# Kernel optimization log

Measured on AMD Instinct MI355X. Metric: run time of the kernel, lower is better.

The kernel has to match this reference:

```python
import jax, jax.numpy as jnp
import numpy as np

V, D, H, L_GNN = 50000, 256, 256, 4
B, NODES_PER_G, L, OUT = 16, 4000, 512, 256
N = B * NODES_PER_G            # 64000 total nodes
E = N * 16                     # 1,024,000 edges (avg degree 16)


def setup_inputs() -> dict:
    key = jax.random.key(0)
    ks = jax.random.split(key, 14)
    s = 0.02  # param init scale
    # per-graph local indices, offset into the flat node array (mirrors the
    # indices[...] + sum(x_len[:i]) reconstruction in the torch code)
    local = jax.random.randint(ks[3], (B, L), 0, NODES_PER_G)
    offsets = (jnp.arange(B, dtype=jnp.int32) * NODES_PER_G)[:, None]
    return {
        "x": jax.random.randint(ks[0], (N,), 0, V, dtype=jnp.int32),
        "edge_index": jax.random.randint(ks[1], (2, E), 0, N, dtype=jnp.int32),
        "edge_weight": jax.random.uniform(ks[2], (E,), jnp.float32),
        "gather_idx": (local + offsets).astype(jnp.int32),
        "mask": jnp.ones((B, L), dtype=bool),
        "encoder_embed": jax.random.normal(ks[4], (B, L, H), jnp.float32),
        "emb": jax.random.normal(ks[5], (V, D), jnp.float32) * s,
        "ggc_w": jax.random.normal(ks[6], (L_GNN, H, H), jnp.float32) * s,
        "w_ih": jax.random.normal(ks[7], (3 * H, H), jnp.float32) * s,
        "w_hh": jax.random.normal(ks[8], (3 * H, H), jnp.float32) * s,
        "b_ih": jnp.zeros((3 * H,), jnp.float32),
        "b_hh": jnp.zeros((3 * H,), jnp.float32),
        "out_w": jax.random.normal(ks[9], (OUT, 2 * H), jnp.float32) * s,
        "out_b": jnp.zeros((OUT,), jnp.float32),
    }


def _gru_cell(m, h, w_ih, w_hh, b_ih, b_hh):
    # torch.nn.GRUCell, gate order (r, z, n)
    gi = m @ w_ih.T + b_ih          # [N, 3H]
    gh = h @ w_hh.T + b_hh
    i_r, i_z, i_n = jnp.split(gi, 3, axis=-1)
    h_r, h_z, h_n = jnp.split(gh, 3, axis=-1)
    r = jax.nn.sigmoid(i_r + h_r)
    z = jax.nn.sigmoid(i_z + h_z)
    n = jnp.tanh(i_n + r * h_n)
    return (1.0 - z) * n + z * h


def reference(x, edge_index, edge_weight, gather_idx, mask, encoder_embed,
              emb, ggc_w, w_ih, w_hh, b_ih, b_hh, out_w, out_b):
    src, dst = edge_index[0], edge_index[1]  # PyG: aggregate x_j at target i
    h = emb[x]                                # [N, H] (dropout=0 -> identity)
    for i in range(L_GNN):                    # GatedGraphConv
        m = h @ ggc_w[i]                      # [N, H]
        msg = m[src] * edge_weight[:, None]   # [E, H]
        agg = jax.ops.segment_sum(msg, dst, num_segments=N)
        h = _gru_cell(agg, h, w_ih, w_hh, b_ih, b_hh)
    # gather per-graph node outputs and zero-pad to max_node_len
    out = h[gather_idx] * mask[:, :, None].astype(h.dtype)  # [B, L, H]
    out = jnp.concatenate([out, encoder_embed], axis=-1)    # [B, L, 2H]
    return out @ out_w.T + out_b                            # [B, L, OUT]
```

## Files before the change

kernel.cpp:

```cpp
#include <hip/hip_runtime.h>
#include <hip/hip_bf16.h>

typedef __hip_bfloat16 bf16;
typedef unsigned short u16;
typedef __attribute__((ext_vector_type(8))) short s8v;
typedef __attribute__((ext_vector_type(4))) float f4v;

#define MFMA16(a, b, c) __builtin_amdgcn_mfma_f32_16x16x32_bf16((a), (b), (c), 0, 0, 0)

__device__ __forceinline__ float b2f(bf16 v) { return __bfloat162float(v); }
__device__ __forceinline__ float sigm(float x) { return 1.0f / (1.0f + __expf(-x)); }
__device__ __forceinline__ float u2f(u16 u) {
  union { float f; unsigned int i; } v; v.i = ((unsigned int)u) << 16; return v.f;
}
__device__ __forceinline__ u16 f2u(float f) {
  bf16 b = __float2bfloat16(f);
  union { bf16 b; u16 u; } v; v.b = b; return v.u;
}

__device__ __forceinline__ void gl16(void* lds, const void* g) {
  __builtin_amdgcn_global_load_lds(
      (const __attribute__((address_space(1))) unsigned int*)g,
      (__attribute__((address_space(3))) unsigned int*)lds, 16, 0, 0);
}

__global__ __launch_bounds__(256) void k_cast(const float* __restrict__ s,
                                              bf16* __restrict__ d, int n) {
  int i = blockIdx.x * 256 + threadIdx.x;
  if (i < n) d[i] = __float2bfloat16(s[i]);
}

__global__ __launch_bounds__(256) void k_embed(const int* __restrict__ x,
                                               const float* __restrict__ emb,
                                               bf16* __restrict__ h, int N, int H) {
  int idx = blockIdx.x * 256 + threadIdx.x;
  if (idx >= N * H) return;
  int n = idx / H, c = idx - n * H;
  h[idx] = __float2bfloat16(emb[(size_t)x[n] * H + c]);
}

__global__ __launch_bounds__(256) void k_cat(const bf16* __restrict__ h,
                                             const int* __restrict__ gidx,
                                             const float* __restrict__ enc,
                                             bf16* __restrict__ catA, int BL, int H) {
  int i = blockIdx.x * 256 + threadIdx.x;
  if (i >= BL * 2 * H) return;
  int r = i / (2 * H), k = i - r * 2 * H;
  catA[i] = (k < H) ? h[(size_t)gidx[r] * H + k]
                    : __float2bfloat16(enc[(size_t)r * H + (k - H)]);
}

__global__ __launch_bounds__(256) void k_zero_i32(int* __restrict__ p, int n) {
  int i = blockIdx.x * 256 + threadIdx.x;
  if (i < n) p[i] = 0;
}
__global__ __launch_bounds__(256) void k_hist(const int* __restrict__ ei,
                                              int* __restrict__ deg, int E) {
  int e = blockIdx.x * 256 + threadIdx.x;
  if (e < E) atomicAdd(&deg[ei[E + e]], 1);
}

__global__ __launch_bounds__(256) void k_scan1(const int* __restrict__ deg,
                                               int* __restrict__ bsum, int N) {
  int t = threadIdx.x;
  int i = blockIdx.x * 256 + t;
  int v = (i < N) ? deg[i] : 0;
#pragma unroll
  for (int o = 32; o > 0; o >>= 1) v += __shfl_down(v, o, 64);
  __shared__ int ws[4];
  if ((t & 63) == 0) ws[t >> 6] = v;
  __syncthreads();
  if (t == 0) bsum[blockIdx.x] = ws[0] + ws[1] + ws[2] + ws[3];
}
__global__ __launch_bounds__(256) void k_scan2(const int* __restrict__ bsum,
                                               int* __restrict__ boff, int nb) {
  __shared__ int s[256];
  int t = threadIdx.x;
  int carry = 0;
  for (int base = 0; base < nb; base += 256) {
    int v = (base + t < nb) ? bsum[base + t] : 0;
    s[t] = v;
    __syncthreads();
    for (int o = 1; o < 256; o <<= 1) {
      int u = (t >= o) ? s[t - o] : 0;
      __syncthreads();
      s[t] += u;
      __syncthreads();
    }
    if (base + t < nb) boff[base + t] = carry + s[t] - v;
    carry += s[255];
    __syncthreads();
  }
}
__global__ __launch_bounds__(256) void k_scan3(const int* __restrict__ deg,
                                               const int* __restrict__ boff,
                                               int* __restrict__ rowptr,
                                               int* __restrict__ cursor, int N) {
  __shared__ int s[256];
  int t = threadIdx.x;
  int i = blockIdx.x * 256 + t;
  int v = (i < N) ? deg[i] : 0;
  s[t] = v;
  __syncthreads();
  for (int o = 1; o < 256; o <<= 1) {
    int u = (t >= o) ? s[t - o] : 0;
    __syncthreads();
    s[t] += u;
    __syncthreads();
  }
  int ex = boff[blockIdx.x] + s[t] - v;
  if (i < N) { rowptr[i] = ex; cursor[i] = ex; }
  if (i == N - 1) rowptr[N] = ex + v;
}

__global__ __launch_bounds__(256) void k_fill(const int* __restrict__ ei,
                                              const float* __restrict__ ew,
                                              int* __restrict__ cursor,
                                              int* __restrict__ srcs,
                                              float* __restrict__ wts, int E) {
  int e = blockIdx.x * 256 + threadIdx.x;
  if (e >= E) return;
  int d = ei[E + e];
  int pos = atomicAdd(&cursor[d], 1);
  srcs[pos] = ei[e];
  wts[pos] = ew[e];
}

__global__ __launch_bounds__(256) void k_aggregate(const int* __restrict__ rowptr,
                                                   const int* __restrict__ srcs,
                                                   const float* __restrict__ wts,
                                                   const bf16* __restrict__ hsrc,
                                                   bf16* __restrict__ sh,
                                                   int N, int H) {
  int wv = threadIdx.x >> 6, lane = threadIdx.x & 63;
  int d = blockIdx.x * 4 + wv;
  if (d >= N) return;
  int beg = rowptr[d], end = rowptr[d + 1];
  const u16* hp = (const u16*)hsrc;
  for (int c0 = lane * 4; c0 < H; c0 += 256) {
    float a0 = 0.f, a1 = 0.f, a2 = 0.f, a3 = 0.f;
    int i = beg;
    for (; i + 4 <= end; i += 4) {
      int s0 = srcs[i], s1 = srcs[i + 1], s2 = srcs[i + 2], s3 = srcs[i + 3];
      float w0 = wts[i], w1 = wts[i + 1], w2 = wts[i + 2], w3 = wts[i + 3];
      ushort4 r0 = *(const ushort4*)(hp + (size_t)s0 * H + c0);
      ushort4 r1 = *(const ushort4*)(hp + (size_t)s1 * H + c0);
      ushort4 r2 = *(const ushort4*)(hp + (size_t)s2 * H + c0);
      ushort4 r3 = *(const ushort4*)(hp + (size_t)s3 * H + c0);
      a0 += w0 * u2f(r0.x) + w1 * u2f(r1.x) + w2 * u2f(r2.x) + w3 * u2f(r3.x);
      a1 += w0 * u2f(r0.y) + w1 * u2f(r1.y) + w2 * u2f(r2.y) + w3 * u2f(r3.y);
      a2 += w0 * u2f(r0.z) + w1 * u2f(r1.z) + w2 * u2f(r2.z) + w3 * u2f(r3.z);
      a3 += w0 * u2f(r0.w) + w1 * u2f(r1.w) + w2 * u2f(r2.w) + w3 * u2f(r3.w);
    }
    for (; i < end; i++) {
      int s0 = srcs[i];
      float w0 = wts[i];
      ushort4 r0 = *(const ushort4*)(hp + (size_t)s0 * H + c0);
      a0 += w0 * u2f(r0.x); a1 += w0 * u2f(r0.y);
      a2 += w0 * u2f(r0.z); a3 += w0 * u2f(r0.w);
    }
    ushort4 o;
    o.x = f2u(a0); o.y = f2u(a1); o.z = f2u(a2); o.w = f2u(a3);
    *(ushort4*)((u16*)sh + (size_t)d * H + c0) = o;
  }
}

template <int OUT_F32>
__global__ __launch_bounds__(256) void k_gemm(const bf16* __restrict__ A,
                                              const bf16* __restrict__ Bt,
                                              void* __restrict__ Cv,
                                              const float* __restrict__ bias,
                                              int M, int K, int Nc,
                                              size_t sBt, size_t sC) {
  __shared__ short As[128][40];
  __shared__ short Bs[64][40];
  int gm = blockIdx.x * 128, gn = blockIdx.y * 64;
  Bt += (size_t)blockIdx.z * sBt;
  size_t zc = (size_t)blockIdx.z * sC;
  int tid = threadIdx.x, w = tid >> 6, lane = tid & 63;
  int l15 = lane & 15, koff = (lane >> 4) * 8;
  f4v acc[2][4];
#pragma unroll
  for (int i = 0; i < 2; i++)
#pragma unroll
    for (int j = 0; j < 4; j++) acc[i][j] = (f4v)0.f;

  for (int kt = 0; kt < K; kt += 32) {
#pragma unroll
    for (int c = 0; c < 2; c++) {
      int ch = tid + c * 256;
      int row = ch >> 2, seg = ch & 3;
      *(float4*)&As[row][seg * 8] =
          *(const float4*)(A + (size_t)(gm + row) * K + kt + seg * 8);
    }
    {
      int row = tid >> 2, seg = tid & 3;
      *(float4*)&Bs[row][seg * 8] =
          *(const float4*)(Bt + (size_t)(gn + row) * K + kt + seg * 8);
    }
    __syncthreads();
    s8v af[2], bf[4];
#pragma unroll
    for (int rt = 0; rt < 2; rt++) af[rt] = *(const s8v*)&As[w * 32 + rt * 16 + l15][koff];
#pragma unroll
    for (int ct = 0; ct < 4; ct++) bf[ct] = *(const s8v*)&Bs[ct * 16 + l15][koff];
#pragma unroll
    for (int rt = 0; rt < 2; rt++)
#pragma unroll
      for (int ct = 0; ct < 4; ct++) acc[rt][ct] = MFMA16(af[rt], bf[ct], acc[rt][ct]);
    __syncthreads();
  }
#pragma unroll
  for (int rt = 0; rt < 2; rt++)
#pragma unroll
    for (int ct = 0; ct < 4; ct++)
#pragma unroll
      for (int r = 0; r < 4; r++) {
        int row = gm + w * 32 + rt * 16 + (lane >> 4) * 4 + r;
        int col = gn + ct * 16 + l15;
        float v = acc[rt][ct][r];
        if (OUT_F32) ((float*)Cv)[zc + (size_t)row * Nc + col] = v + bias[col];
        else         ((bf16*)Cv)[zc + (size_t)row * Nc + col] = __float2bfloat16(v);
      }
}

#define GRU_STAGE(Aarr, Harr, Barr, kt)                   \
  {                                                       \
    gl16(&Aarr[tid * 8],            Ap  + (kt));          \
    gl16(&Aarr[2048 + tid * 8],     Ap  + rstep + (kt));  \
    gl16(&Harr[tid * 8],            Hp  + (kt));          \
    gl16(&Harr[2048 + tid * 8],     Hp  + rstep + (kt));  \
    gl16(&Barr[tid * 8],            BiP + (kt));          \
    gl16(&Barr[2048 + tid * 8],     BiP + HH + (kt));     \
    gl16(&Barr[2 * 2048 + tid * 8], BiP + 2 * HH + (kt)); \
    gl16(&Barr[3 * 2048 + tid * 8], BhP + (kt));          \
    gl16(&Barr[4 * 2048 + tid * 8], BhP + HH + (kt));     \
    gl16(&Barr[5 * 2048 + tid * 8], BhP + 2 * HH + (kt)); \
  }

#define GRU_COMPUTE(Aarr, Harr, Barr)                                       \
  {                                                                         \
    s8v fa[2], fh[2];                                                       \
    _Pragma("unroll")                                                       \
    for (int rt = 0; rt < 2; rt++) {                                        \
      fa[rt] = *(const s8v*)&Aarr[(w * 32 + rt * 16 + l15) * 32 + koff];    \
      fh[rt] = *(const s8v*)&Harr[(w * 32 + rt * 16 + l15) * 32 + koff];    \
    }                                                                       \
    _Pragma("unroll")                                                       \
    for (int ct = 0; ct < 4; ct++) {                                        \
      int brow = (ct * 16 + l15) * 32 + koff;                               \
      s8v bRi = *(const s8v*)&Barr[brow];                                   \
      s8v bZi = *(const s8v*)&Barr[2048 + brow];                            \
      s8v bNi = *(const s8v*)&Barr[2 * 2048 + brow];                        \
      s8v bRh = *(const s8v*)&Barr[3 * 2048 + brow];                        \
      s8v bZh = *(const s8v*)&Barr[4 * 2048 + brow];                        \
      s8v bNh = *(const s8v*)&Barr[5 * 2048 + brow];                        \
      _Pragma("unroll")                                                     \
      for (int rt = 0; rt < 2; rt++) {                                      \
        accR[rt][ct]  = MFMA16(fa[rt], bRi, accR[rt][ct]);                  \
        accR[rt][ct]  = MFMA16(fh[rt], bRh, accR[rt][ct]);                  \
        accZ[rt][ct]  = MFMA16(fa[rt], bZi, accZ[rt][ct]);                  \
        accZ[rt][ct]  = MFMA16(fh[rt], bZh, accZ[rt][ct]);                  \
        accNi[rt][ct] = MFMA16(fa[rt], bNi, accNi[rt][ct]);                 \
        accNh[rt][ct] = MFMA16(fh[rt], bNh, accNh[rt][ct]);                 \
      }                                                                     \
    }                                                                       \
  }

__global__ __launch_bounds__(256, 2) void k_gru_mfma(const bf16* __restrict__ Ash,
                                                     const bf16* __restrict__ Ah,
                                                     const bf16* __restrict__ Wi,
                                                     const bf16* __restrict__ Wh,
                                                     const float* __restrict__ bi,
                                                     const float* __restrict__ bh,
                                                     bf16* __restrict__ hn,
                                                     int M, int H) {
  __shared__ __align__(16) short Aa0[128 * 32], Aa1[128 * 32];
  __shared__ __align__(16) short Hs0[128 * 32], Hs1[128 * 32];
  __shared__ __align__(16) short Bs0[6 * 64 * 32], Bs1[6 * 64 * 32];

  int nwgx = H >> 6;
  int nwg = gridDim.x;
  int bid = blockIdx.x;
  int wg = bid;
  if ((nwg & 7) == 0) { int cpx = nwg >> 3; wg = (bid & 7) * cpx + (bid >> 3); }
  int gcol = (wg % nwgx) * 64;
  int gm = (wg / nwgx) * 128;

  int tid = threadIdx.x, w = tid >> 6, lane = tid & 63;
  int l15 = lane & 15, koff = (lane >> 4) * 8;
  f4v accR[2][4], accZ[2][4], accNi[2][4], accNh[2][4];
#pragma unroll
  for (int rt = 0; rt < 2; rt++)
#pragma unroll
    for (int ct = 0; ct < 4; ct++) {
      accR[rt][ct] = (f4v)0.f; accZ[rt][ct] = (f4v)0.f;
      accNi[rt][ct] = (f4v)0.f; accNh[rt][ct] = (f4v)0.f;
    }

  int arow = tid >> 2, aseg = tid & 3;
  const bf16* Ap  = Ash + (size_t)(gm + arow) * H + aseg * 8;
  const bf16* Hp  = Ah  + (size_t)(gm + arow) * H + aseg * 8;
  const bf16* BiP = Wi  + (size_t)(gcol + arow) * H + aseg * 8;
  const bf16* BhP = Wh  + (size_t)(gcol + arow) * H + aseg * 8;
  size_t HH = (size_t)H * H;
  size_t rstep = (size_t)64 * H;

  int nk = H >> 5;
  GRU_STAGE(Aa0, Hs0, Bs0, 0);
  __syncthreads();
  for (int t = 0; t < nk; t += 2) {
    int kt = t << 5;
    if (t + 1 < nk) GRU_STAGE(Aa1, Hs1, Bs1, kt + 32);
    GRU_COMPUTE(Aa0, Hs0, Bs0);
    __syncthreads();
    if (t + 2 < nk) GRU_STAGE(Aa0, Hs0, Bs0, kt + 64);
    if (t + 1 < nk) GRU_COMPUTE(Aa1, Hs1, Bs1);
    __syncthreads();
  }

#pragma unroll
  for (int ct = 0; ct < 4; ct++) {
    int col = gcol + ct * 16 + l15;
    float br  = bi[col] + bh[col];
    float bz  = bi[H + col] + bh[H + col];
    float bin = bi[2 * H + col], bhn = bh[2 * H + col];
#pragma unroll
    for (int rt = 0; rt < 2; rt++)
#pragma unroll
      for (int r = 0; r < 4; r++) {
        int row = gm + w * 32 + rt * 16 + (lane >> 4) * 4 + r;
        float rr = sigm(accR[rt][ct][r] + br);
        float zz = sigm(accZ[rt][ct][r] + bz);
        float nn = tanhf(accNi[rt][ct][r] + bin + rr * (accNh[rt][ct][r] + bhn));
        float hv = b2f(Ah[(size_t)row * H + col]);
        hn[(size_t)row * H + col] = __float2bfloat16((1.f - zz) * nn + zz * hv);
      }
  }
}

static inline size_t alg(size_t x) { return (x + 255) & ~(size_t)255; }
static inline int cdiv(int a, int b) { return (a + b - 1) / b; }

extern "C" void kernel_launch(void* const* d_in, const int* in_sizes, int n_in,
                              void* d_out, int out_size, void* d_ws, size_t ws_size,
                              hipStream_t stream) {
  (void)out_size; (void)ws_size;
  int s = (n_in >= 14) ? 0 : -1;
  const int*   x     = (const int*)d_in[0];
  const int*   ei    = (const int*)d_in[1];
  const float* ew    = (const float*)d_in[2];
  const int*   gidx  = (const int*)d_in[3];
  const float* enc   = (const float*)d_in[5 + s];
  const float* emb   = (const float*)d_in[6 + s];
  const float* ggcw  = (const float*)d_in[7 + s];
  const float* w_ih  = (const float*)d_in[8 + s];
  const float* w_hh  = (const float*)d_in[9 + s];
  const float* b_ih  = (const float*)d_in[10 + s];
  const float* b_hh  = (const float*)d_in[11 + s];
  const float* out_w = (const float*)d_in[12 + s];
  const float* out_b = (const float*)d_in[13 + s];
  float* out = (float*)d_out;

  int N   = in_sizes[0];
  int E   = in_sizes[2];
  int BL  = in_sizes[3];
  int H   = in_sizes[5 + s] / BL;
  int LG  = in_sizes[7 + s] / (H * H);
  int OUT = in_sizes[12 + s] / (2 * H);

  size_t nh = (size_t)N * H;
  size_t hh3 = (size_t)3 * H * H;
  int nb = cdiv(N, 256);
  char* p = (char*)d_ws;
  size_t off = 0;
  bf16* wihB  = (bf16*)(p + off); off = alg(off + hh3 * 2);
  bf16* whhB  = (bf16*)(p + off); off = alg(off + hh3 * 2);
  bf16* outwB = (bf16*)(p + off); off = alg(off + (size_t)OUT * 2 * H * 2);
  bf16* ggcwB = (bf16*)(p + off); off = alg(off + (size_t)LG * H * H * 2);
  bf16* Ucomb = (bf16*)(p + off); off = alg(off + (size_t)LG * hh3 * 2);
  bf16* hA    = (bf16*)(p + off); off = alg(off + nh * 2);
  bf16* hB    = (bf16*)(p + off); off = alg(off + nh * 2);
  bf16* shB   = (bf16*)(p + off); off = alg(off + nh * 2);
  bf16* catA  = (bf16*)(p + off); off = alg(off + (size_t)BL * 2 * H * 2);
  int* deg    = (int*)(p + off);  off = alg(off + (size_t)N * 4);
  int* rowptr = (int*)(p + off);  off = alg(off + (size_t)(N + 1) * 4);
  int* cursor = (int*)(p + off);  off = alg(off + (size_t)N * 4);
  int* srcs   = (int*)(p + off);  off = alg(off + (size_t)E * 4);
  float* wts  = (float*)(p + off); off = alg(off + (size_t)E * 4);
  int* bsum   = (int*)(p + off);  off = alg(off + (size_t)nb * 4);
  int* boff   = (int*)(p + off);  off = alg(off + (size_t)nb * 4);

  k_cast<<<cdiv((int)hh3, 256), 256, 0, stream>>>(w_ih, wihB, (int)hh3);
  k_cast<<<cdiv((int)hh3, 256), 256, 0, stream>>>(w_hh, whhB, (int)hh3);
  k_cast<<<cdiv(OUT * 2 * H, 256), 256, 0, stream>>>(out_w, outwB, OUT * 2 * H);
  k_cast<<<cdiv(LG * H * H, 256), 256, 0, stream>>>(ggcw, ggcwB, LG * H * H);
  k_gemm<0><<<dim3(3 * H / 128, H / 64, LG), 256, 0, stream>>>(
      wihB, ggcwB, Ucomb, nullptr, 3 * H, H, H, (size_t)H * H, hh3);

  k_embed<<<cdiv(N * H, 256), 256, 0, stream>>>(x, emb, hA, N, H);
  k_zero_i32<<<cdiv(N, 256), 256, 0, stream>>>(deg, N);
  k_hist<<<cdiv(E, 256), 256, 0, stream>>>(ei, deg, E);
  k_scan1<<<nb, 256, 0, stream>>>(deg, bsum, N);
  k_scan2<<<1, 256, 0, stream>>>(bsum, boff, nb);
  k_scan3<<<nb, 256, 0, stream>>>(deg, boff, rowptr, cursor, N);
  k_fill<<<cdiv(E, 256), 256, 0, stream>>>(ei, ew, cursor, srcs, wts, E);

  bf16* h = hA;
  bf16* hn = hB;
  for (int l = 0; l < LG; l++) {
    k_aggregate<<<cdiv(N, 4), 256, 0, stream>>>(rowptr, srcs, wts, h, shB, N, H);
    k_gru_mfma<<<dim3((H / 64) * (N / 128)), 256, 0, stream>>>(
        shB, h, Ucomb + (size_t)l * hh3, whhB, b_ih, b_hh, hn, N, H);
    bf16* t = h; h = hn; hn = t;
  }
  k_cat<<<cdiv(BL * 2 * H, 256), 256, 0, stream>>>(h, gidx, enc, catA, BL, H);
  k_gemm<1><<<dim3(BL / 128, OUT / 64, 1), 256, 0, stream>>>(
      catA, outwB, out, out_b, BL, 2 * H, OUT, 0, 0);
}
```

Before: 909.6 us.

## Load GRU A/H operands directly into registers, drop their LDS staging

New measurement: 1.319 ms. +45.0%, slower.

```diff
diff --git a/kernel.cpp b/kernel.cpp
--- a/kernel.cpp
+++ b/kernel.cpp
@@ -224,12 +224,8 @@
       }
 }
 
-#define GRU_STAGE(Aarr, Harr, Barr, kt)                   \
+#define GRU_STAGE_B(Barr, kt)                             \
   {                                                       \
-    gl16(&Aarr[tid * 8],            Ap  + (kt));          \
-    gl16(&Aarr[2048 + tid * 8],     Ap  + rstep + (kt));  \
-    gl16(&Harr[tid * 8],            Hp  + (kt));          \
-    gl16(&Harr[2048 + tid * 8],     Hp  + rstep + (kt));  \
     gl16(&Barr[tid * 8],            BiP + (kt));          \
     gl16(&Barr[2048 + tid * 8],     BiP + HH + (kt));     \
     gl16(&Barr[2 * 2048 + tid * 8], BiP + 2 * HH + (kt)); \
@@ -238,14 +234,16 @@
     gl16(&Barr[5 * 2048 + tid * 8], BhP + 2 * HH + (kt)); \
   }
 
-#define GRU_COMPUTE(Aarr, Harr, Barr)                                       \
+#define GRU_LOADA(fa, fh, kt)                             \
+  {                                                       \
+    fa[0] = *(const s8v*)(ApF + (kt));                    \
+    fa[1] = *(const s8v*)(ApF + rtF + (kt));              \
+    fh[0] = *(const s8v*)(HpF + (kt));                    \
+    fh[1] = *(const s8v*)(HpF + rtF + (kt));              \
+  }
+
+#define GRU_COMPUTE(Barr, fa, fh)                                           \
   {                                                                         \
-    s8v fa[2], fh[2];                                                       \
-    _Pragma("unroll")                                                       \
-    for (int rt = 0; rt < 2; rt++) {                                        \
-      fa[rt] = *(const s8v*)&Aarr[(w * 32 + rt * 16 + l15) * 32 + koff];    \
-      fh[rt] = *(const s8v*)&Harr[(w * 32 + rt * 16 + l15) * 32 + koff];    \
-    }                                                                       \
     _Pragma("unroll")                                                       \
     for (int ct = 0; ct < 4; ct++) {                                        \
       int brow = (ct * 16 + l15) * 32 + koff;                               \
@@ -267,7 +265,7 @@
     }                                                                       \
   }
 
-__global__ __launch_bounds__(256, 2) void k_gru_mfma(const bf16* __restrict__ Ash,
+__global__ __launch_bounds__(256, 3) void k_gru_mfma(const bf16* __restrict__ Ash,
                                                      const bf16* __restrict__ Ah,
                                                      const bf16* __restrict__ Wi,
                                                      const bf16* __restrict__ Wh,
@@ -275,8 +273,6 @@
                                                      const float* __restrict__ bh,
                                                      bf16* __restrict__ hn,
                                                      int M, int H) {
-  __shared__ __align__(16) short Aa0[128 * 32], Aa1[128 * 32];
-  __shared__ __align__(16) short Hs0[128 * 32], Hs1[128 * 32];
   __shared__ __align__(16) short Bs0[6 * 64 * 32], Bs1[6 * 64 * 32];
 
   int nwgx = H >> 6;
@@ -299,23 +295,27 @@
     }
 
   int arow = tid >> 2, aseg = tid & 3;
-  const bf16* Ap  = Ash + (size_t)(gm + arow) * H + aseg * 8;
-  const bf16* Hp  = Ah  + (size_t)(gm + arow) * H + aseg * 8;
-  const bf16* BiP = Wi  + (size_t)(gcol + arow) * H + aseg * 8;
-  const bf16* BhP = Wh  + (size_t)(gcol + arow) * H + aseg * 8;
+  const bf16* BiP = Wi + (size_t)(gcol + arow) * H + aseg * 8;
+  const bf16* BhP = Wh + (size_t)(gcol + arow) * H + aseg * 8;
   size_t HH = (size_t)H * H;
-  size_t rstep = (size_t)64 * H;
+
+  const bf16* ApF = Ash + (size_t)(gm + w * 32 + l15) * H + koff;
+  const bf16* HpF = Ah  + (size_t)(gm + w * 32 + l15) * H + koff;
+  size_t rtF = (size_t)16 * H;
 
   int nk = H >> 5;
-  GRU_STAGE(Aa0, Hs0, Bs0, 0);
+  s8v faA[2], fhA[2], faB[2], fhB[2];
+
+  GRU_STAGE_B(Bs0, 0);
+  GRU_LOADA(faA, fhA, 0);
   __syncthreads();
   for (int t = 0; t < nk; t += 2) {
     int kt = t << 5;
-    if (t + 1 < nk) GRU_STAGE(Aa1, Hs1, Bs1, kt + 32);
-    GRU_COMPUTE(Aa0, Hs0, Bs0);
-    __syncthreads();
-    if (t + 2 < nk) GRU_STAGE(Aa0, Hs0, Bs0, kt + 64);
-    if (t + 1 < nk) GRU_COMPUTE(Aa1, Hs1, Bs1);
+    if (t + 1 < nk) { GRU_STAGE_B(Bs1, kt + 32); GRU_LOADA(faB, fhB, kt + 32); }
+    GRU_COMPUTE(Bs0, faA, fhA);
+    __syncthreads();
+    if (t + 2 < nk) { GRU_STAGE_B(Bs0, kt + 64); GRU_LOADA(faA, fhA, kt + 64); }
+    if (t + 1 < nk) GRU_COMPUTE(Bs1, faB, fhB);
     __syncthreads();
   }
 
```
